# Performance work log

Measured on AMD Instinct MI355X. Metric: run time of the kernel, lower is better.

The kernel has to match this reference:

```python
import jax, jax.numpy as jnp
import numpy as np

NITER = 100
ALPHA = 0.3
SIGMA = 32768.0  # N / 2
PDIST_EPS = 1e-6  # torch.nn.PairwiseDistance default eps


def setup_inputs() -> dict:
    key = jax.random.key(0)
    k1, k2 = jax.random.split(key)
    N, dim = 65536, 1024
    x = jax.random.normal(k1, (dim,), dtype=jnp.float32)
    weights = jax.random.normal(k2, (N, dim), dtype=jnp.float32)
    locations = jnp.arange(N, dtype=jnp.int32)
    return {"x": x, "weights": weights, "locations": locations, "it": 10}


def reference(x, weights, locations, it):
    # Pairwise L2 distance of single input against all N prototypes
    diff = x[None, :] - weights + PDIST_EPS          # (N, dim)
    dists = jnp.sqrt(jnp.sum(diff * diff, axis=1))   # (N,)
    bmu_index = jnp.argmin(dists)                    # scalar int

    lr = 1.0 - it / NITER
    alpha_op = ALPHA * lr
    sigma_op = SIGMA * lr

    # Gaussian neighbourhood on the 1-D grid of neuron locations
    bmu_dist_sq = jnp.square((locations - bmu_index).astype(jnp.float32))  # (N,)
    neighbourhood = jnp.exp(-bmu_dist_sq / (sigma_op ** 2))                # (N,)
    lr_mult = (alpha_op * neighbourhood)[:, None]                          # (N, 1)

    delta = lr_mult * (x[None, :] - weights)         # (N, dim)
    new_weights = weights + delta
    return new_weights
```

## Files before the change

kernel.cpp:

```cpp
#include <hip/hip_runtime.h>
#include <stdint.h>


#define N_ROWS 65536
#define DIM    1024
#define EPS    1e-6f
#define NITER  100.0f
#define ALPHA  0.3f
#define SIGMA  32768.0f

#define DIST_BLOCKS 2048
#define ROWS_PER_WAVE (N_ROWS / (DIST_BLOCKS * 4))

__global__ __launch_bounds__(256) void som_dist(
    const float* __restrict__ x,
    const float* __restrict__ w,
    unsigned long long* __restrict__ part)
{
    const int lane = threadIdx.x & 63;
    const int wave = threadIdx.x >> 6;
    const int waveGlobal = blockIdx.x * 4 + wave;
    const int row0 = waveGlobal * ROWS_PER_WAVE;

    const float4* xv4 = (const float4*)x;

    unsigned long long best = ~0ull;

    for (int r = 0; r < ROWS_PER_WAVE; ++r) {
        const int row = row0 + r;
        const float4* wr = (const float4*)(w + (size_t)row * DIM);
        float s = 0.0f;
        #pragma unroll
        for (int p = 0; p < 4; ++p) {
            float4 wv = wr[p * 64 + lane];
            float4 xx = xv4[p * 64 + lane];
            float t;
            t = xx.x - wv.x + EPS; s = fmaf(t, t, s);
            t = xx.y - wv.y + EPS; s = fmaf(t, t, s);
            t = xx.z - wv.z + EPS; s = fmaf(t, t, s);
            t = xx.w - wv.w + EPS; s = fmaf(t, t, s);
        }
        #pragma unroll
        for (int off = 32; off > 0; off >>= 1)
            s += __shfl_down(s, off, 64);
        if (lane == 0) {
            float d = sqrtf(s);
            unsigned long long enc =
                ((unsigned long long)__float_as_uint(d) << 32) | (unsigned)row;
            best = best < enc ? best : enc;
        }
    }

    __shared__ unsigned long long sm[4];
    if (lane == 0) sm[wave] = best;
    __syncthreads();
    if (threadIdx.x == 0) {
        unsigned long long b = sm[0];
        #pragma unroll
        for (int i = 1; i < 4; ++i) b = b < sm[i] ? b : sm[i];
        part[blockIdx.x] = b;
    }
}

__global__ __launch_bounds__(256) void som_reduce(unsigned long long* __restrict__ part)
{
    __shared__ unsigned long long sm[256];
    unsigned long long b = ~0ull;
    for (int i = threadIdx.x; i < DIST_BLOCKS; i += 256) {
        unsigned long long v = part[i];
        b = b < v ? b : v;
    }
    sm[threadIdx.x] = b;
    __syncthreads();
    #pragma unroll
    for (int s = 128; s > 0; s >>= 1) {
        if (threadIdx.x < s) {
            unsigned long long v = sm[threadIdx.x + s];
            if (v < sm[threadIdx.x]) sm[threadIdx.x] = v;
        }
        __syncthreads();
    }
    if (threadIdx.x == 0) part[DIST_BLOCKS] = sm[0];
}

__global__ __launch_bounds__(256) void som_update(
    const float* __restrict__ x,
    const float* __restrict__ w,
    const int* __restrict__ loc,
    const int* __restrict__ itp,
    const unsigned long long* __restrict__ winner,
    float* __restrict__ out)
{
    const int i = blockIdx.x * 256 + threadIdx.x;
    const int row  = i >> 8;
    const int col4 = i & 255;

    const int bmu = (int)(unsigned)(winner[DIST_BLOCKS] & 0xffffffffull);

    const float lr       = 1.0f - (float)itp[0] / NITER;
    const float alpha_op = ALPHA * lr;
    const float sigma_op = SIGMA * lr;
    const float inv_s2   = 1.0f / (sigma_op * sigma_op);

    const float dloc  = (float)(loc[row] - bmu);
    const float neigh = expf(-(dloc * dloc) * inv_s2);
    const float lrm   = alpha_op * neigh;

    const float4 wv = ((const float4*)(w + (size_t)row * DIM))[col4];
    const float4 xx = ((const float4*)x)[col4];

    float4 o;
    o.x = fmaf(lrm, xx.x - wv.x, wv.x);
    o.y = fmaf(lrm, xx.y - wv.y, wv.y);
    o.z = fmaf(lrm, xx.z - wv.z, wv.z);
    o.w = fmaf(lrm, xx.w - wv.w, wv.w);

    ((float4*)(out + (size_t)row * DIM))[col4] = o;
}

extern "C" void kernel_launch(void* const* d_in, const int* in_sizes, int n_in,
                              void* d_out, int out_size, void* d_ws, size_t ws_size,
                              hipStream_t stream)
{
    const float* x  = (const float*)d_in[0];
    const float* w  = (const float*)d_in[1];
    const int* loc  = (const int*)d_in[2];
    const int* itp  = (const int*)d_in[3];
    float* out      = (float*)d_out;
    unsigned long long* part = (unsigned long long*)d_ws;

    som_dist<<<DIST_BLOCKS, 256, 0, stream>>>(x, w, part);
    som_reduce<<<1, 256, 0, stream>>>(part);

    const int total4 = N_ROWS * (DIM / 4);
    som_update<<<total4 / 256, 256, 0, stream>>>(x, w, loc, itp, part, out);
}
```

Baseline: 487.7 us.

## Batch distance rows, hoist x loads, and loop update blocks in reverse with nontemporal stores

After: 491.9 us. Within noise of the previous version (+0.9%).

```diff
diff --git a/kernel.cpp b/kernel.cpp
--- a/kernel.cpp
+++ b/kernel.cpp
@@ -5,12 +5,24 @@
 #define N_ROWS 65536
 #define DIM    1024
 #define EPS    1e-6f
-#define NITER  100.0f
+#define NITERF 100.0f
 #define ALPHA  0.3f
 #define SIGMA  32768.0f
 
-#define DIST_BLOCKS 2048
+#define DIST_BLOCKS   1024
 #define ROWS_PER_WAVE (N_ROWS / (DIST_BLOCKS * 4))
+#define BATCH         4
+
+#define UPD_BLOCKS    2048
+#define ROWS_PER_UBLK (N_ROWS / UPD_BLOCKS)
+
+typedef float nfloat4 __attribute__((ext_vector_type(4)));
+
+#define ACC4(XX, WW) \
+    t = XX.x - WW.x + EPS; s = fmaf(t, t, s); \
+    t = XX.y - WW.y + EPS; s = fmaf(t, t, s); \
+    t = XX.z - WW.z + EPS; s = fmaf(t, t, s); \
+    t = XX.w - WW.w + EPS; s = fmaf(t, t, s);
 
 __global__ __launch_bounds__(256) void som_dist(
     const float* __restrict__ x,
@@ -19,35 +31,48 @@
 {
     const int lane = threadIdx.x & 63;
     const int wave = threadIdx.x >> 6;
-    const int waveGlobal = blockIdx.x * 4 + wave;
-    const int row0 = waveGlobal * ROWS_PER_WAVE;
+    const int waveRow0 = (blockIdx.x * 4 + wave) * ROWS_PER_WAVE;
 
     const float4* xv4 = (const float4*)x;
+    const float4 xx0 = xv4[0 * 64 + lane];
+    const float4 xx1 = xv4[1 * 64 + lane];
+    const float4 xx2 = xv4[2 * 64 + lane];
+    const float4 xx3 = xv4[3 * 64 + lane];
 
     unsigned long long best = ~0ull;
 
-    for (int r = 0; r < ROWS_PER_WAVE; ++r) {
-        const int row = row0 + r;
-        const float4* wr = (const float4*)(w + (size_t)row * DIM);
-        float s = 0.0f;
+    for (int b = 0; b < ROWS_PER_WAVE; b += BATCH) {
+        float acc[BATCH];
         #pragma unroll
-        for (int p = 0; p < 4; ++p) {
-            float4 wv = wr[p * 64 + lane];
-            float4 xx = xv4[p * 64 + lane];
-            float t;
-            t = xx.x - wv.x + EPS; s = fmaf(t, t, s);
-            t = xx.y - wv.y + EPS; s = fmaf(t, t, s);
-            t = xx.z - wv.z + EPS; s = fmaf(t, t, s);
-            t = xx.w - wv.w + EPS; s = fmaf(t, t, s);
+        for (int r = 0; r < BATCH; ++r) {
+            const int row = waveRow0 + b + r;
+            const float4* wr = (const float4*)(w + (size_t)row * DIM);
+            float4 w0 = wr[0 * 64 + lane];
+            float4 w1 = wr[1 * 64 + lane];
+            float4 w2 = wr[2 * 64 + lane];
+            float4 w3 = wr[3 * 64 + lane];
+            float s = 0.0f, t;
+            ACC4(xx0, w0)
+            ACC4(xx1, w1)
+            ACC4(xx2, w2)
+            ACC4(xx3, w3)
+            acc[r] = s;
         }
         #pragma unroll
-        for (int off = 32; off > 0; off >>= 1)
-            s += __shfl_down(s, off, 64);
+        for (int off = 32; off > 0; off >>= 1) {
+            #pragma unroll
+            for (int r = 0; r < BATCH; ++r)
+                acc[r] += __shfl_down(acc[r], off, 64);
+        }
         if (lane == 0) {
-            float d = sqrtf(s);
-            unsigned long long enc =
-                ((unsigned long long)__float_as_uint(d) << 32) | (unsigned)row;
-            best = best < enc ? best : enc;
+            #pragma unroll
+            for (int r = 0; r < BATCH; ++r) {
+                float d = sqrtf(acc[r]);
+                unsigned long long enc =
+                    ((unsigned long long)__float_as_uint(d) << 32) |
+                    (unsigned)(waveRow0 + b + r);
+                best = best < enc ? best : enc;
+            }
         }
     }
 
@@ -55,10 +80,10 @@
     if (lane == 0) sm[wave] = best;
     __syncthreads();
     if (threadIdx.x == 0) {
-        unsigned long long b = sm[0];
+        unsigned long long v = sm[0];
         #pragma unroll
-        for (int i = 1; i < 4; ++i) b = b < sm[i] ? b : sm[i];
-        part[blockIdx.x] = b;
+        for (int i = 1; i < 4; ++i) v = v < sm[i] ? v : sm[i];
+        part[blockIdx.x] = v;
     }
 }
 
@@ -91,31 +116,33 @@
     const unsigned long long* __restrict__ winner,
     float* __restrict__ out)
 {
-    const int i = blockIdx.x * 256 + threadIdx.x;
-    const int row  = i >> 8;
-    const int col4 = i & 255;
+    const int tid = threadIdx.x;
+    const int blk  = (UPD_BLOCKS - 1) - blockIdx.x;
+    const int row0 = blk * ROWS_PER_UBLK;
 
     const int bmu = (int)(unsigned)(winner[DIST_BLOCKS] & 0xffffffffull);
 
-    const float lr       = 1.0f - (float)itp[0] / NITER;
+    const float lr       = 1.0f - (float)itp[0] / NITERF;
     const float alpha_op = ALPHA * lr;
     const float sigma_op = SIGMA * lr;
     const float inv_s2   = 1.0f / (sigma_op * sigma_op);
 
-    const float dloc  = (float)(loc[row] - bmu);
-    const float neigh = expf(-(dloc * dloc) * inv_s2);
-    const float lrm   = alpha_op * neigh;
+    const float4 xq = ((const float4*)x)[tid];
 
-    const float4 wv = ((const float4*)(w + (size_t)row * DIM))[col4];
-    const float4 xx = ((const float4*)x)[col4];
+    for (int r = ROWS_PER_UBLK - 1; r >= 0; --r) {
+        const int row = row0 + r;
+        const float dloc  = (float)(loc[row] - bmu);
+        const float neigh = expf(-(dloc * dloc) * inv_s2);
+        const float lrm   = alpha_op * neigh;
 
-    float4 o;
-    o.x = fmaf(lrm, xx.x - wv.x, wv.x);
-    o.y = fmaf(lrm, xx.y - wv.y, wv.y);
-    o.z = fmaf(lrm, xx.z - wv.z, wv.z);
-    o.w = fmaf(lrm, xx.w - wv.w, wv.w);
-
-    ((float4*)(out + (size_t)row * DIM))[col4] = o;
+        const float4 wv = ((const float4*)(w + (size_t)row * DIM))[tid];
+        nfloat4 o;
+        o.x = fmaf(lrm, xq.x - wv.x, wv.x);
+        o.y = fmaf(lrm, xq.y - wv.y, wv.y);
+        o.z = fmaf(lrm, xq.z - wv.z, wv.z);
+        o.w = fmaf(lrm, xq.w - wv.w, wv.w);
+        __builtin_nontemporal_store(o, (nfloat4*)(out + (size_t)row * DIM) + tid);
+    }
 }
 
 extern "C" void kernel_launch(void* const* d_in, const int* in_sizes, int n_in,
@@ -131,7 +158,5 @@
 
     som_dist<<<DIST_BLOCKS, 256, 0, stream>>>(x, w, part);
     som_reduce<<<1, 256, 0, stream>>>(part);
-
-    const int total4 = N_ROWS * (DIM / 4);
-    som_update<<<total4 / 256, 256, 0, stream>>>(x, w, loc, itp, part, out);
+    som_update<<<UPD_BLOCKS, 256, 0, stream>>>(x, w, loc, itp, part, out);
 }
```
